# Kernel tuning notes

Measured on AMD Instinct MI355X. Metric: run time of the kernel, lower is better.

The kernel has to match this reference:

```python
import jax, jax.numpy as jnp
import numpy as np

SIGMA_X = 1.0
SIGMA_Y = 1.0
MASK_DENSITY = 0.001


def _gauss_kernel(n, sigma):
    # K[a, b] = exp(-(a - b)^2 / (2 sigma^2)), shape (n, n)
    c = jnp.arange(n, dtype=jnp.float32)
    d = c[:, None] - c[None, :]
    return jnp.exp(-(d * d) / (2.0 * sigma * sigma))


def setup_inputs() -> dict:
    key = jax.random.key(0)
    k1, k2 = jax.random.split(key)
    B, C, H, W = 32, 4, 512, 512
    x = jax.random.normal(k1, (B, C, H, W), dtype=jnp.float32)
    # channel 2 is a sparse binary target mask (the module calls nonzero on it)
    mask = (jax.random.uniform(k2, (B, H, W)) < MASK_DENSITY).astype(jnp.float32)
    x = x.at[:, 2, :, :].set(mask)
    return {"x": x}


def reference(x):
    # Faithful to Preprocessor.forward: replace channel 2 with a max-normalized
    # sum of unit-amplitude Gaussians centered at every pixel where ch2 > 0.
    # The per-point scatter-add of full (H,W) Gaussians is mathematically a
    # separable dense convolution of the 0/1 indicator with the Gaussian kernel:
    #   G[b,h,w] = sum_{i,j} 1[ch2[b,i,j] > 0] * exp(-(h-i)^2/(2 sx^2)) * exp(-(w-j)^2/(2 sy^2))
    B, C, H, W = x.shape
    ch2 = x[:, 2, :, :]
    ind = (ch2 > 0).astype(x.dtype)  # (B, H, W), indicator (not the values)
    Kx = _gauss_kernel(H, SIGMA_X).astype(x.dtype)  # (H, H)
    Ky = _gauss_kernel(W, SIGMA_Y).astype(x.dtype)  # (W, W)
    G = jnp.einsum("hi,bij,jw->bhw", Kx, ind, Ky)
    m = jnp.max(G.reshape(B, -1), axis=1).reshape(B, 1, 1)
    m = jnp.where(m == 0, jnp.ones_like(m), m)  # max==0 -> divide by 1
    G = G / m
    return x.at[:, 2, :, :].set(G)
```

## Files before the change

### kernel.cpp

```cpp
#include <hip/hip_runtime.h>

static constexpr int   Bn   = 32;
static constexpr int   Hn   = 512;
static constexpr int   Wn   = 512;
static constexpr int   HWn  = Hn * Wn;
static constexpr int   PL4  = HWn / 4;
static constexpr int   CAP  = 1024;
static constexpr int   RAD  = 7;
static constexpr int   WIN  = 2 * RAD + 1;
static constexpr float SIGMA_X = 1.0f;
static constexpr float SIGMA_Y = 1.0f;

typedef float vf4 __attribute__((ext_vector_type(4)));


__global__ __launch_bounds__(256) void k_copy_detect(
    const vf4* __restrict__ x, vf4* __restrict__ out,
    int* __restrict__ counts, int* __restrict__ coords)
{
    const int N4 = Bn * 4 * PL4;
    const int stride = gridDim.x * 256;
    const int lane = threadIdx.x & 63;
    const unsigned long long lt = (1ull << lane) - 1ull;
    for (int i = blockIdx.x * 256 + threadIdx.x; i < N4; i += stride) {
        vf4 v = x[i];
        int pi = i >> 16;
        if ((pi & 3) == 2) {
            vf4 z = {0.f, 0.f, 0.f, 0.f};
            out[i] = z;
            unsigned long long m0 = __ballot(v.x > 0.f);
            unsigned long long m1 = __ballot(v.y > 0.f);
            unsigned long long m2 = __ballot(v.z > 0.f);
            unsigned long long m3 = __ballot(v.w > 0.f);
            int c0 = __popcll(m0), c1 = __popcll(m1), c2 = __popcll(m2), c3 = __popcll(m3);
            int tot = c0 + c1 + c2 + c3;
            if (tot) {
                int b  = pi >> 2;
                int hw = (i & (PL4 - 1)) * 4;
                int base = 0;
                if (lane == 0) base = atomicAdd(&counts[b * 32], tot);
                base = __shfl(base, 0, 64);
                int* cb = coords + b * CAP;
                if (v.x > 0.f) { int k = base + __popcll(m0 & lt);                 if (k < CAP) cb[k] = hw;     }
                if (v.y > 0.f) { int k = base + c0 + __popcll(m1 & lt);            if (k < CAP) cb[k] = hw + 1; }
                if (v.z > 0.f) { int k = base + c0 + c1 + __popcll(m2 & lt);       if (k < CAP) cb[k] = hw + 2; }
                if (v.w > 0.f) { int k = base + c0 + c1 + c2 + __popcll(m3 & lt);  if (k < CAP) cb[k] = hw + 3; }
            }
        } else {
            out[i] = v;
        }
    }
}

__global__ __launch_bounds__(256) void k_scatter_max(
    const int* __restrict__ counts, const int* __restrict__ coords,
    float* __restrict__ out, unsigned int* __restrict__ m)
{
    __shared__ float wx[WIN], wy[WIN];
    if (threadIdx.x < WIN) {
        float d = (float)((int)threadIdx.x - RAD);
        wx[threadIdx.x] = expf(-(d * d) / (2.f * SIGMA_X * SIGMA_X));
        wy[threadIdx.x] = expf(-(d * d) / (2.f * SIGMA_Y * SIGMA_Y));
    }
    __syncthreads();

    int b = blockIdx.x;
    int n = counts[b * 32]; if (n > CAP) n = CAP;
    float* g = out + ((size_t)b * 4 + 2) * HWn;
    int total  = n * (WIN * WIN);
    int stride = gridDim.y * blockDim.x;
    float mx = 0.f;
    for (int idx = blockIdx.y * blockDim.x + threadIdx.x; idx < total; idx += stride) {
        int p    = idx / (WIN * WIN);
        int cell = idx - p * (WIN * WIN);
        int c  = coords[b * CAP + p];
        int i  = c >> 9;
        int j  = c & (Wn - 1);
        int dh = cell / WIN;
        int dw = cell - dh * WIN;
        int h  = i + dh - RAD;
        int w  = j + dw - RAD;
        if ((unsigned)h < (unsigned)Hn && (unsigned)w < (unsigned)Wn) {
            float wgt = wx[dh] * wy[dw];
            float old = atomicAdd(&g[h * Wn + w], wgt);
            mx = fmaxf(mx, old + wgt);
        }
    }
    for (int o = 32; o > 0; o >>= 1) mx = fmaxf(mx, __shfl_down(mx, o));
    __shared__ float smx[4];
    if ((threadIdx.x & 63) == 0) smx[threadIdx.x >> 6] = mx;
    __syncthreads();
    if (threadIdx.x == 0) {
        mx = fmaxf(fmaxf(smx[0], smx[1]), fmaxf(smx[2], smx[3]));
        atomicMax(&m[b * 32], __float_as_uint(mx));
    }
}

__global__ __launch_bounds__(256) void k_norm(
    vf4* __restrict__ out, const unsigned int* __restrict__ m)
{
    int t = blockIdx.x * 256 + threadIdx.x;
    int b = t >> 16;
    int q = t & (PL4 - 1);
    float mv = __uint_as_float(m[b * 32]);
    float s  = (mv == 0.f) ? 1.f : 1.f / mv;
    vf4* g = out + ((size_t)b * 4 + 2) * PL4;
    vf4 v = g[q];
    v.x *= s; v.y *= s; v.z *= s; v.w *= s;
    g[q] = v;
}

extern "C" void kernel_launch(void* const* d_in, const int* in_sizes, int n_in,
                              void* d_out, int out_size, void* d_ws, size_t ws_size,
                              hipStream_t stream) {
    const float* x = (const float*)d_in[0];
    float* out = (float*)d_out;

    int*          counts = (int*)d_ws;
    unsigned int* m      = (unsigned int*)d_ws + 1024;
    int*          coords = (int*)d_ws + 2048;

    (void)hipMemsetAsync(d_ws, 0, 2048 * sizeof(int), stream);

    k_copy_detect<<<2048, 256, 0, stream>>>((const vf4*)x, (vf4*)out, counts, coords);
    k_scatter_max<<<dim3(Bn, 8), 256, 0, stream>>>(counts, coords, out, m);
    k_norm       <<<Bn * PL4 / 256, 256, 0, stream>>>((vf4*)out, m);
}
```

Before: 270.1 us.

## Replace atomic scatter with spatially binned gather evaluation of Gaussian field

Points are sorted into 16x16-pixel spatial bins, and channel 2 is computed by gathering contributions from nearby bins per pixel instead of scattering with global atomics. The max is computed separately by evaluating the field only at pixels covered by point windows. The output is then written directly with normalization applied, which removes the zero-fill, atomic scatter and read-modify-write normalization passes. The copy of the other channels is split into its own kernel. In exchange there are more kernel launches and a per-bin capacity of 8 points that silently drops any excess, and the write kernel runs a per-pixel gather loop over up to 4 bins.

After: 468.8 us. 73.6% more time.

```diff
diff --git a/kernel.cpp b/kernel.cpp
--- a/kernel.cpp
+++ b/kernel.cpp
@@ -8,83 +8,132 @@
 static constexpr int   CAP  = 1024;
 static constexpr int   RAD  = 7;
 static constexpr int   WIN  = 2 * RAD + 1;
+static constexpr int   BINS = 32;
+static constexpr int   NCELL= BINS * BINS;
+static constexpr int   BCAP = 8;
 static constexpr float SIGMA_X = 1.0f;
 static constexpr float SIGMA_Y = 1.0f;
 
 typedef float vf4 __attribute__((ext_vector_type(4)));
 
 
-__global__ __launch_bounds__(256) void k_copy_detect(
-    const vf4* __restrict__ x, vf4* __restrict__ out,
-    int* __restrict__ counts, int* __restrict__ coords)
-{
-    const int N4 = Bn * 4 * PL4;
-    const int stride = gridDim.x * 256;
+__global__ __launch_bounds__(256) void k_copy013(
+    const vf4* __restrict__ x, vf4* __restrict__ out)
+{
+    int t  = blockIdx.x * 256 + threadIdx.x;
+    int pc = t >> 16;
+    int q  = t & 65535;
+    int b  = pc / 3;
+    int ci = pc - b * 3;
+    int c  = ci + (ci >> 1);
+    size_t idx = ((size_t)(b * 4 + c) << 16) + q;
+    out[idx] = x[idx];
+}
+
+__global__ __launch_bounds__(256) void k_detect(
+    const vf4* __restrict__ x, int* __restrict__ counts, int* __restrict__ coords)
+{
+    int t = blockIdx.x * 256 + threadIdx.x;
+    int b = t >> 16;
+    int q = t & 65535;
+    vf4 v = x[((size_t)(b * 4 + 2) << 16) + q];
     const int lane = threadIdx.x & 63;
     const unsigned long long lt = (1ull << lane) - 1ull;
-    for (int i = blockIdx.x * 256 + threadIdx.x; i < N4; i += stride) {
-        vf4 v = x[i];
-        int pi = i >> 16;
-        if ((pi & 3) == 2) {
-            vf4 z = {0.f, 0.f, 0.f, 0.f};
-            out[i] = z;
-            unsigned long long m0 = __ballot(v.x > 0.f);
-            unsigned long long m1 = __ballot(v.y > 0.f);
-            unsigned long long m2 = __ballot(v.z > 0.f);
-            unsigned long long m3 = __ballot(v.w > 0.f);
-            int c0 = __popcll(m0), c1 = __popcll(m1), c2 = __popcll(m2), c3 = __popcll(m3);
-            int tot = c0 + c1 + c2 + c3;
-            if (tot) {
-                int b  = pi >> 2;
-                int hw = (i & (PL4 - 1)) * 4;
-                int base = 0;
-                if (lane == 0) base = atomicAdd(&counts[b * 32], tot);
-                base = __shfl(base, 0, 64);
-                int* cb = coords + b * CAP;
-                if (v.x > 0.f) { int k = base + __popcll(m0 & lt);                 if (k < CAP) cb[k] = hw;     }
-                if (v.y > 0.f) { int k = base + c0 + __popcll(m1 & lt);            if (k < CAP) cb[k] = hw + 1; }
-                if (v.z > 0.f) { int k = base + c0 + c1 + __popcll(m2 & lt);       if (k < CAP) cb[k] = hw + 2; }
-                if (v.w > 0.f) { int k = base + c0 + c1 + c2 + __popcll(m3 & lt);  if (k < CAP) cb[k] = hw + 3; }
+    unsigned long long m0 = __ballot(v.x > 0.f);
+    unsigned long long m1 = __ballot(v.y > 0.f);
+    unsigned long long m2 = __ballot(v.z > 0.f);
+    unsigned long long m3 = __ballot(v.w > 0.f);
+    int c0 = __popcll(m0), c1 = __popcll(m1), c2 = __popcll(m2), c3 = __popcll(m3);
+    int tot = c0 + c1 + c2 + c3;
+    if (tot) {
+        int hw = q * 4;
+        int base = 0;
+        if (lane == 0) base = atomicAdd(&counts[b * 32], tot);
+        base = __shfl(base, 0, 64);
+        int* cb = coords + b * CAP;
+        if (v.x > 0.f) { int k = base + __popcll(m0 & lt);                if (k < CAP) cb[k] = hw;     }
+        if (v.y > 0.f) { int k = base + c0 + __popcll(m1 & lt);           if (k < CAP) cb[k] = hw + 1; }
+        if (v.z > 0.f) { int k = base + c0 + c1 + __popcll(m2 & lt);      if (k < CAP) cb[k] = hw + 2; }
+        if (v.w > 0.f) { int k = base + c0 + c1 + c2 + __popcll(m3 & lt); if (k < CAP) cb[k] = hw + 3; }
+    }
+}
+
+__global__ __launch_bounds__(256) void k_bin(
+    const int* __restrict__ counts, const int* __restrict__ coords,
+    int* __restrict__ bincnt, int* __restrict__ binlist)
+{
+    int b = blockIdx.x;
+    int* bc = bincnt + b * NCELL;
+    for (int i = threadIdx.x; i < NCELL; i += 256) bc[i] = 0;
+    __syncthreads();
+    int n = counts[b * 32]; if (n > CAP) n = CAP;
+    for (int p = threadIdx.x; p < n; p += 256) {
+        int c = coords[b * CAP + p];
+        int cell = ((c >> 9) >> 4) * BINS + ((c & 511) >> 4);
+        int k = atomicAdd(&bc[cell], 1);
+        if (k < BCAP) binlist[(b * NCELL + cell) * BCAP + k] = c;
+    }
+}
+
+__device__ __forceinline__ float eval_px(
+    int h, int w, const int* s_bincnt, const int* s_binlist,
+    const float* swx, const float* swy)
+{
+    float val = 0.f;
+    int bh0 = (h - RAD) >> 4; if (bh0 < 0) bh0 = 0;
+    int bh1 = (h + RAD) >> 4; if (bh1 > BINS - 1) bh1 = BINS - 1;
+    int bw0 = (w - RAD) >> 4; if (bw0 < 0) bw0 = 0;
+    int bw1 = (w + RAD) >> 4; if (bw1 > BINS - 1) bw1 = BINS - 1;
+    for (int bh = bh0; bh <= bh1; ++bh)
+        for (int bw = bw0; bw <= bw1; ++bw) {
+            int cell = bh * BINS + bw;
+            int cnt = s_bincnt[cell];
+            for (int k = 0; k < cnt; ++k) {
+                int c  = s_binlist[cell * BCAP + k];
+                int di = h - (c >> 9) + RAD;
+                int dj = w - (c & 511) + RAD;
+                if ((unsigned)di < (unsigned)WIN && (unsigned)dj < (unsigned)WIN)
+                    val += swx[di] * swy[dj];
             }
-        } else {
-            out[i] = v;
         }
-    }
-}
-
-__global__ __launch_bounds__(256) void k_scatter_max(
+    return val;
+}
+
+__global__ __launch_bounds__(256) void k_max(
     const int* __restrict__ counts, const int* __restrict__ coords,
-    float* __restrict__ out, unsigned int* __restrict__ m)
-{
-    __shared__ float wx[WIN], wy[WIN];
+    const int* __restrict__ bincnt, const int* __restrict__ binlist,
+    unsigned int* __restrict__ m)
+{
+    __shared__ float swx[WIN], swy[WIN];
+    __shared__ int s_bincnt[NCELL];
+    __shared__ int s_binlist[NCELL * BCAP];
+    int b = blockIdx.x;
     if (threadIdx.x < WIN) {
         float d = (float)((int)threadIdx.x - RAD);
-        wx[threadIdx.x] = expf(-(d * d) / (2.f * SIGMA_X * SIGMA_X));
-        wy[threadIdx.x] = expf(-(d * d) / (2.f * SIGMA_Y * SIGMA_Y));
-    }
-    __syncthreads();
-
-    int b = blockIdx.x;
+        swx[threadIdx.x] = expf(-(d * d) / (2.f * SIGMA_X * SIGMA_X));
+        swy[threadIdx.x] = expf(-(d * d) / (2.f * SIGMA_Y * SIGMA_Y));
+    }
+    for (int i = threadIdx.x; i < NCELL; i += 256) {
+        int cnt = bincnt[b * NCELL + i];
+        s_bincnt[i] = (cnt > BCAP) ? BCAP : cnt;
+    }
+    for (int i = threadIdx.x; i < NCELL * BCAP; i += 256)
+        s_binlist[i] = binlist[b * NCELL * BCAP + i];
+    __syncthreads();
+
     int n = counts[b * 32]; if (n > CAP) n = CAP;
-    float* g = out + ((size_t)b * 4 + 2) * HWn;
-    int total  = n * (WIN * WIN);
-    int stride = gridDim.y * blockDim.x;
+    int total = n * (WIN * WIN);
     float mx = 0.f;
-    for (int idx = blockIdx.y * blockDim.x + threadIdx.x; idx < total; idx += stride) {
+    for (int idx = blockIdx.y * 256 + threadIdx.x; idx < total; idx += gridDim.y * 256) {
         int p    = idx / (WIN * WIN);
         int cell = idx - p * (WIN * WIN);
         int c  = coords[b * CAP + p];
-        int i  = c >> 9;
-        int j  = c & (Wn - 1);
         int dh = cell / WIN;
         int dw = cell - dh * WIN;
-        int h  = i + dh - RAD;
-        int w  = j + dw - RAD;
-        if ((unsigned)h < (unsigned)Hn && (unsigned)w < (unsigned)Wn) {
-            float wgt = wx[dh] * wy[dw];
-            float old = atomicAdd(&g[h * Wn + w], wgt);
-            mx = fmaxf(mx, old + wgt);
-        }
+        int h  = (c >> 9) + dh - RAD;
+        int w  = (c & 511) + dw - RAD;
+        if ((unsigned)h < (unsigned)Hn && (unsigned)w < (unsigned)Wn)
+            mx = fmaxf(mx, eval_px(h, w, s_bincnt, s_binlist, swx, swy));
     }
     for (int o = 32; o > 0; o >>= 1) mx = fmaxf(mx, __shfl_down(mx, o));
     __shared__ float smx[4];
@@ -96,18 +145,41 @@
     }
 }
 
-__global__ __launch_bounds__(256) void k_norm(
-    vf4* __restrict__ out, const unsigned int* __restrict__ m)
-{
-    int t = blockIdx.x * 256 + threadIdx.x;
-    int b = t >> 16;
-    int q = t & (PL4 - 1);
+__global__ __launch_bounds__(256) void k_write2(
+    const unsigned int* __restrict__ m, const int* __restrict__ bincnt,
+    const int* __restrict__ binlist, vf4* __restrict__ out)
+{
+    __shared__ float swx[WIN], swy[WIN];
+    __shared__ int s_bincnt[NCELL];
+    __shared__ int s_binlist[NCELL * BCAP];
+    int b = blockIdx.x;
+    if (threadIdx.x < WIN) {
+        float d = (float)((int)threadIdx.x - RAD);
+        swx[threadIdx.x] = expf(-(d * d) / (2.f * SIGMA_X * SIGMA_X));
+        swy[threadIdx.x] = expf(-(d * d) / (2.f * SIGMA_Y * SIGMA_Y));
+    }
+    for (int i = threadIdx.x; i < NCELL; i += 256) {
+        int cnt = bincnt[b * NCELL + i];
+        s_bincnt[i] = (cnt > BCAP) ? BCAP : cnt;
+    }
+    for (int i = threadIdx.x; i < NCELL * BCAP; i += 256)
+        s_binlist[i] = binlist[b * NCELL * BCAP + i];
+    __syncthreads();
+
     float mv = __uint_as_float(m[b * 32]);
     float s  = (mv == 0.f) ? 1.f : 1.f / mv;
-    vf4* g = out + ((size_t)b * 4 + 2) * PL4;
-    vf4 v = g[q];
-    v.x *= s; v.y *= s; v.z *= s; v.w *= s;
-    g[q] = v;
+    vf4* g = out + ((size_t)(b * 4 + 2) << 16);
+    for (int q = blockIdx.y * 256 + threadIdx.x; q < PL4; q += gridDim.y * 256) {
+        int pix = q * 4;
+        int h  = pix >> 9;
+        int w0 = pix & 511;
+        vf4 r;
+        r.x = eval_px(h, w0 + 0, s_bincnt, s_binlist, swx, swy) * s;
+        r.y = eval_px(h, w0 + 1, s_bincnt, s_binlist, swx, swy) * s;
+        r.z = eval_px(h, w0 + 2, s_bincnt, s_binlist, swx, swy) * s;
+        r.w = eval_px(h, w0 + 3, s_bincnt, s_binlist, swx, swy) * s;
+        g[q] = r;
+    }
 }
 
 extern "C" void kernel_launch(void* const* d_in, const int* in_sizes, int n_in,
@@ -116,13 +188,17 @@
     const float* x = (const float*)d_in[0];
     float* out = (float*)d_out;
 
-    int*          counts = (int*)d_ws;
-    unsigned int* m      = (unsigned int*)d_ws + 1024;
-    int*          coords = (int*)d_ws + 2048;
+    int*          counts  = (int*)d_ws;
+    unsigned int* m       = (unsigned int*)d_ws + 1024;
+    int*          coords  = (int*)d_ws + 2048;
+    int*          bincnt  = (int*)d_ws + 34816;
+    int*          binlist = (int*)d_ws + 67584;
 
     (void)hipMemsetAsync(d_ws, 0, 2048 * sizeof(int), stream);
 
-    k_copy_detect<<<2048, 256, 0, stream>>>((const vf4*)x, (vf4*)out, counts, coords);
-    k_scatter_max<<<dim3(Bn, 8), 256, 0, stream>>>(counts, coords, out, m);
-    k_norm       <<<Bn * PL4 / 256, 256, 0, stream>>>((vf4*)out, m);
-}
+    k_copy013<<<96 * PL4 / 256, 256, 0, stream>>>((const vf4*)x, (vf4*)out);
+    k_detect <<<Bn * PL4 / 256, 256, 0, stream>>>((const vf4*)x, counts, coords);
+    k_bin    <<<Bn, 256, 0, stream>>>(counts, coords, bincnt, binlist);
+    k_max    <<<dim3(Bn, 2),  256, 0, stream>>>(counts, coords, bincnt, binlist, m);
+    k_write2 <<<dim3(Bn, 16), 256, 0, stream>>>(m, bincnt, binlist, (vf4*)out);
+}
```

## Replace atomic scatter with binned gather-based tile evaluation of Gaussians

Applied to the files above, without the earlier changes.

Points are binned into 16x16 spatial cells during the copy pass. The atomic scatter-add is replaced by per-32x32-tile gather kernels that evaluate the Gaussian sum from nearby bins twice, once for the max and once to write the normalized output. This removes the zero-fill and re-read/write normalization pass over channel 2, as well as the global float atomics. In exchange the Gaussian is computed twice, and bins are capped at 8 points, so dense regions could drop points.

Measured after the change: 255.5 us. -5.4%, faster.

```diff
diff --git a/kernel.cpp b/kernel.cpp
--- a/kernel.cpp
+++ b/kernel.cpp
@@ -5,9 +5,12 @@
 static constexpr int   Wn   = 512;
 static constexpr int   HWn  = Hn * Wn;
 static constexpr int   PL4  = HWn / 4;
-static constexpr int   CAP  = 1024;
 static constexpr int   RAD  = 7;
 static constexpr int   WIN  = 2 * RAD + 1;
+static constexpr int   BINS = 32;
+static constexpr int   NCELL= BINS * BINS;
+static constexpr int   BCAP = 8;
+static constexpr int   MSLOT= 8;
 static constexpr float SIGMA_X = 1.0f;
 static constexpr float SIGMA_Y = 1.0f;
 
@@ -16,98 +19,153 @@
 
 __global__ __launch_bounds__(256) void k_copy_detect(
     const vf4* __restrict__ x, vf4* __restrict__ out,
-    int* __restrict__ counts, int* __restrict__ coords)
+    int* __restrict__ bincnt, int* __restrict__ binlist)
 {
     const int N4 = Bn * 4 * PL4;
-    const int stride = gridDim.x * 256;
-    const int lane = threadIdx.x & 63;
-    const unsigned long long lt = (1ull << lane) - 1ull;
-    for (int i = blockIdx.x * 256 + threadIdx.x; i < N4; i += stride) {
-        vf4 v = x[i];
-        int pi = i >> 16;
-        if ((pi & 3) == 2) {
-            vf4 z = {0.f, 0.f, 0.f, 0.f};
-            out[i] = z;
-            unsigned long long m0 = __ballot(v.x > 0.f);
-            unsigned long long m1 = __ballot(v.y > 0.f);
-            unsigned long long m2 = __ballot(v.z > 0.f);
-            unsigned long long m3 = __ballot(v.w > 0.f);
-            int c0 = __popcll(m0), c1 = __popcll(m1), c2 = __popcll(m2), c3 = __popcll(m3);
-            int tot = c0 + c1 + c2 + c3;
-            if (tot) {
-                int b  = pi >> 2;
-                int hw = (i & (PL4 - 1)) * 4;
-                int base = 0;
-                if (lane == 0) base = atomicAdd(&counts[b * 32], tot);
-                base = __shfl(base, 0, 64);
-                int* cb = coords + b * CAP;
-                if (v.x > 0.f) { int k = base + __popcll(m0 & lt);                 if (k < CAP) cb[k] = hw;     }
-                if (v.y > 0.f) { int k = base + c0 + __popcll(m1 & lt);            if (k < CAP) cb[k] = hw + 1; }
-                if (v.z > 0.f) { int k = base + c0 + c1 + __popcll(m2 & lt);       if (k < CAP) cb[k] = hw + 2; }
-                if (v.w > 0.f) { int k = base + c0 + c1 + c2 + __popcll(m3 & lt);  if (k < CAP) cb[k] = hw + 3; }
+    const int NT = 2048 * 256;
+    const int t  = blockIdx.x * 256 + threadIdx.x;
+    const int pi0 = t >> 16;
+    if ((pi0 & 3) != 2) {
+        for (int i = t; i < N4; i += NT)
+            out[i] = x[i];
+    } else {
+        for (int i = t; i < N4; i += NT) {
+            vf4 v = x[i];
+            int nh = (v.x > 0.f) + (v.y > 0.f) + (v.z > 0.f) + (v.w > 0.f);
+            if (nh) {
+                int b  = i >> 18;
+                int hw = (i & 65535) * 4;
+                int h  = hw >> 9;
+                int w0 = hw & 511;
+                int cell = b * NCELL + (h >> 4) * BINS + (w0 >> 4);
+                int k = atomicAdd(&bincnt[cell], nh);
+                int* bl = binlist + cell * BCAP;
+                if (v.x > 0.f) { if (k < BCAP) bl[k] = hw;     k++; }
+                if (v.y > 0.f) { if (k < BCAP) bl[k] = hw + 1; k++; }
+                if (v.z > 0.f) { if (k < BCAP) bl[k] = hw + 2; k++; }
+                if (v.w > 0.f) { if (k < BCAP) bl[k] = hw + 3; k++; }
             }
-        } else {
-            out[i] = v;
         }
     }
 }
 
-__global__ __launch_bounds__(256) void k_scatter_max(
-    const int* __restrict__ counts, const int* __restrict__ coords,
-    float* __restrict__ out, unsigned int* __restrict__ m)
+__device__ __forceinline__ void collect_pts(
+    int b, int tr, int tc, const int* __restrict__ bincnt,
+    const int* __restrict__ binlist, int* s_pts, int* s_np)
 {
-    __shared__ float wx[WIN], wy[WIN];
+    if (threadIdx.x < 16) {
+        int bh = 2 * tr - 1 + ((int)threadIdx.x >> 2);
+        int bw = 2 * tc - 1 + ((int)threadIdx.x & 3);
+        if ((unsigned)bh < (unsigned)BINS && (unsigned)bw < (unsigned)BINS) {
+            int cell = b * NCELL + bh * BINS + bw;
+            int cnt = bincnt[cell]; if (cnt > BCAP) cnt = BCAP;
+            if (cnt) {
+                int base = atomicAdd(s_np, cnt);
+                for (int k = 0; k < cnt; ++k)
+                    s_pts[base + k] = binlist[cell * BCAP + k];
+            }
+        }
+    }
+}
+
+__device__ __forceinline__ vf4 eval4(
+    int h, int w0, int np, const int* s_pts, const float* swx, const float* swy)
+{
+    vf4 val = {0.f, 0.f, 0.f, 0.f};
+    for (int p = 0; p < np; ++p) {
+        int c  = s_pts[p];
+        int di = h  - (c >> 9)  + RAD;
+        int dj = w0 - (c & 511) + RAD;
+        if ((unsigned)di < (unsigned)WIN) {
+            float fx = swx[di];
+            if ((unsigned)(dj    ) < (unsigned)WIN) val.x += fx * swy[dj];
+            if ((unsigned)(dj + 1) < (unsigned)WIN) val.y += fx * swy[dj + 1];
+            if ((unsigned)(dj + 2) < (unsigned)WIN) val.z += fx * swy[dj + 2];
+            if ((unsigned)(dj + 3) < (unsigned)WIN) val.w += fx * swy[dj + 3];
+        }
+    }
+    return val;
+}
+
+__global__ __launch_bounds__(256) void k_tile_max(
+    const int* __restrict__ bincnt, const int* __restrict__ binlist,
+    unsigned int* __restrict__ m)
+{
+    __shared__ float swx[WIN], swy[WIN];
+    __shared__ int s_pts[16 * BCAP];
+    __shared__ int s_np;
+    int b    = blockIdx.x >> 8;
+    int tile = blockIdx.x & 255;
+    int tr   = tile >> 4, tc = tile & 15;
+    if (threadIdx.x == 0) s_np = 0;
     if (threadIdx.x < WIN) {
         float d = (float)((int)threadIdx.x - RAD);
-        wx[threadIdx.x] = expf(-(d * d) / (2.f * SIGMA_X * SIGMA_X));
-        wy[threadIdx.x] = expf(-(d * d) / (2.f * SIGMA_Y * SIGMA_Y));
+        swx[threadIdx.x] = expf(-(d * d) / (2.f * SIGMA_X * SIGMA_X));
+        swy[threadIdx.x] = expf(-(d * d) / (2.f * SIGMA_Y * SIGMA_Y));
     }
     __syncthreads();
+    collect_pts(b, tr, tc, bincnt, binlist, s_pts, &s_np);
+    __syncthreads();
+    int np = s_np;
+    if (np == 0) return;
 
-    int b = blockIdx.x;
-    int n = counts[b * 32]; if (n > CAP) n = CAP;
-    float* g = out + ((size_t)b * 4 + 2) * HWn;
-    int total  = n * (WIN * WIN);
-    int stride = gridDim.y * blockDim.x;
-    float mx = 0.f;
-    for (int idx = blockIdx.y * blockDim.x + threadIdx.x; idx < total; idx += stride) {
-        int p    = idx / (WIN * WIN);
-        int cell = idx - p * (WIN * WIN);
-        int c  = coords[b * CAP + p];
-        int i  = c >> 9;
-        int j  = c & (Wn - 1);
-        int dh = cell / WIN;
-        int dw = cell - dh * WIN;
-        int h  = i + dh - RAD;
-        int w  = j + dw - RAD;
-        if ((unsigned)h < (unsigned)Hn && (unsigned)w < (unsigned)Wn) {
-            float wgt = wx[dh] * wy[dw];
-            float old = atomicAdd(&g[h * Wn + w], wgt);
-            mx = fmaxf(mx, old + wgt);
-        }
-    }
+    int r  = threadIdx.x >> 3;
+    int c4 = threadIdx.x & 7;
+    int h  = tr * 32 + r;
+    int w0 = tc * 32 + c4 * 4;
+    vf4 v = eval4(h, w0, np, s_pts, swx, swy);
+    float mx = fmaxf(fmaxf(v.x, v.y), fmaxf(v.z, v.w));
     for (int o = 32; o > 0; o >>= 1) mx = fmaxf(mx, __shfl_down(mx, o));
     __shared__ float smx[4];
     if ((threadIdx.x & 63) == 0) smx[threadIdx.x >> 6] = mx;
     __syncthreads();
     if (threadIdx.x == 0) {
         mx = fmaxf(fmaxf(smx[0], smx[1]), fmaxf(smx[2], smx[3]));
-        atomicMax(&m[b * 32], __float_as_uint(mx));
+        atomicMax(&m[(b * MSLOT + (blockIdx.x & (MSLOT - 1))) * 32],
+                  __float_as_uint(mx));
     }
 }
 
-__global__ __launch_bounds__(256) void k_norm(
-    vf4* __restrict__ out, const unsigned int* __restrict__ m)
+__global__ __launch_bounds__(256) void k_tile_write(
+    const int* __restrict__ bincnt, const int* __restrict__ binlist,
+    const unsigned int* __restrict__ m, vf4* __restrict__ out)
 {
-    int t = blockIdx.x * 256 + threadIdx.x;
-    int b = t >> 16;
-    int q = t & (PL4 - 1);
-    float mv = __uint_as_float(m[b * 32]);
-    float s  = (mv == 0.f) ? 1.f : 1.f / mv;
-    vf4* g = out + ((size_t)b * 4 + 2) * PL4;
-    vf4 v = g[q];
+    __shared__ float swx[WIN], swy[WIN];
+    __shared__ int s_pts[16 * BCAP];
+    __shared__ int s_np;
+    int b    = blockIdx.x >> 8;
+    int tile = blockIdx.x & 255;
+    int tr   = tile >> 4, tc = tile & 15;
+    if (threadIdx.x == 0) s_np = 0;
+    if (threadIdx.x < WIN) {
+        float d = (float)((int)threadIdx.x - RAD);
+        swx[threadIdx.x] = expf(-(d * d) / (2.f * SIGMA_X * SIGMA_X));
+        swy[threadIdx.x] = expf(-(d * d) / (2.f * SIGMA_Y * SIGMA_Y));
+    }
+    __syncthreads();
+    collect_pts(b, tr, tc, bincnt, binlist, s_pts, &s_np);
+    __syncthreads();
+    int np = s_np;
+
+    int r  = threadIdx.x >> 3;
+    int c4 = threadIdx.x & 7;
+    int h  = tr * 32 + r;
+    vf4* g = out + ((size_t)(b * 4 + 2) << 16);
+    int  off = h * (Wn / 4) + tc * 8 + c4;
+    if (np == 0) {
+        vf4 z = {0.f, 0.f, 0.f, 0.f};
+        g[off] = z;
+        return;
+    }
+    float mv = 0.f;
+    #pragma unroll
+    for (int j = 0; j < MSLOT; ++j)
+        mv = fmaxf(mv, __uint_as_float(m[(b * MSLOT + j) * 32]));
+    float s = (mv == 0.f) ? 1.f : 1.f / mv;
+    int w0 = tc * 32 + c4 * 4;
+    vf4 v = eval4(h, w0, np, s_pts, swx, swy);
     v.x *= s; v.y *= s; v.z *= s; v.w *= s;
-    g[q] = v;
+    g[off] = v;
 }
 
 extern "C" void kernel_launch(void* const* d_in, const int* in_sizes, int n_in,
@@ -116,13 +174,13 @@
     const float* x = (const float*)d_in[0];
     float* out = (float*)d_out;
 
-    int*          counts = (int*)d_ws;
-    unsigned int* m      = (unsigned int*)d_ws + 1024;
-    int*          coords = (int*)d_ws + 2048;
+    int*          bincnt  = (int*)d_ws;
+    unsigned int* m       = (unsigned int*)d_ws + 32768;
+    int*          binlist = (int*)d_ws + 40960;
 
-    (void)hipMemsetAsync(d_ws, 0, 2048 * sizeof(int), stream);
+    (void)hipMemsetAsync(d_ws, 0, 40960 * sizeof(int), stream);
 
-    k_copy_detect<<<2048, 256, 0, stream>>>((const vf4*)x, (vf4*)out, counts, coords);
-    k_scatter_max<<<dim3(Bn, 8), 256, 0, stream>>>(counts, coords, out, m);
-    k_norm       <<<Bn * PL4 / 256, 256, 0, stream>>>((vf4*)out, m);
+    k_copy_detect<<<2048, 256, 0, stream>>>((const vf4*)x, (vf4*)out, bincnt, binlist);
+    k_tile_max   <<<Bn * 256, 256, 0, stream>>>(bincnt, binlist, m);
+    k_tile_write <<<Bn * 256, 256, 0, stream>>>(bincnt, binlist, m, (vf4*)out);
 }
```
